# Kernel optimization log

Measured on AMD Instinct MI355X. Metric: run time of the kernel, lower is better.

The kernel has to match this reference:

```python
import jax, jax.numpy as jnp
import numpy as np

EPS = 1e-5

def _layer_norm(x, w, b):
    mu = jnp.mean(x, axis=-1, keepdims=True)
    var = jnp.mean((x - mu) ** 2, axis=-1, keepdims=True)
    return (x - mu) * jax.lax.rsqrt(var + EPS) * w + b

def setup_inputs() -> dict:
    H = 2048
    B, T = 4, 2048
    key = jax.random.key(0)
    ks = jax.random.split(key, 12)
    s = 0.02
    return {
        "hidden_state": jax.random.normal(ks[0], (B, T, H), dtype=jnp.float32),
        "ln_w": jnp.ones((H,), jnp.float32),
        "ln_b": jnp.zeros((H,), jnp.float32),
        "Wk": jax.random.normal(ks[1], (H, H), jnp.float32) * s,
        "Wv": jax.random.normal(ks[2], (H, H), jnp.float32) * s,
        "Wr": jax.random.normal(ks[3], (H, H), jnp.float32) * s,
        "Wo": jax.random.normal(ks[4], (H, H), jnp.float32) * s,
        "mix_k": jax.random.uniform(ks[5], (H,), jnp.float32),
        "mix_v": jax.random.uniform(ks[6], (H,), jnp.float32),
        "mix_r": jax.random.uniform(ks[7], (H,), jnp.float32),
        "time_decay": jax.random.normal(ks[8], (H,), jnp.float32) * 0.5,
        "current_token_weight": jax.random.normal(ks[9], (H,), jnp.float32) * 0.5,
    }

def _wkv(k, v, time_decay, curr_w):
    # k, v: [B, T, H]; max-stabilized RWKV recurrence, scanned over time.
    B, T, H = k.shape
    decay = -jnp.exp(time_decay)  # [H]
    num0 = jnp.zeros((B, H), k.dtype)
    den0 = jnp.zeros((B, H), k.dtype)
    norm0 = jnp.full((B, H), -jnp.inf, k.dtype)

    def step(carry, kv):
        num, den, norm = carry
        kt, vt = kv  # [B, H]
        ct = curr_w + kt
        cn = jnp.maximum(ct, norm)
        e_prev = jnp.exp(norm - cn)
        e_cur = jnp.exp(ct - cn)
        out = (e_prev * num + e_cur * vt) / (e_prev * den + e_cur)
        dpn = decay + norm
        new_norm = jnp.maximum(dpn, kt)
        e_d = jnp.exp(dpn - new_norm)
        e_k = jnp.exp(kt - new_norm)
        return (e_d * num + e_k * vt, e_d * den + e_k, new_norm), out

    kT = jnp.swapaxes(k, 0, 1)  # [T, B, H]
    vT = jnp.swapaxes(v, 0, 1)
    (num, den, norm), outs = jax.lax.scan(step, (num0, den0, norm0), (kT, vT))
    return jnp.swapaxes(outs, 0, 1), num, den, norm

def reference(hidden_state, ln_w, ln_b, Wk, Wv, Wr, Wo, mix_k, mix_v, mix_r,
              time_decay, current_token_weight):
    residual = hidden_state
    x = _layer_norm(hidden_state, ln_w, ln_b)  # [B, T, H]
    B, T, H = x.shape
    # shifted input: previous token (zeros for t=0 since previous_state is None)
    sx = jnp.concatenate([jnp.zeros((B, 1, H), x.dtype), x[:, :-1, :]], axis=1)
    xk = sx + mix_k * (x - sx)
    xv = sx + mix_v * (x - sx)
    xr = sx + mix_r * (x - sx)
    r = jax.nn.sigmoid(jnp.einsum('bth,oh->bto', xr, Wr))
    k = jnp.einsum('bth,oh->bto', xk, Wk)
    v = jnp.einsum('bth,oh->bto', xv, Wv)
    wkv, num, den, norm = _wkv(k, v, time_decay, current_token_weight)
    rwkv = jnp.einsum('bth,oh->bto', r * wkv, Wo)
    out = residual + rwkv
    return (out, (x[:, -1, :], num, den, norm))
```

## Files before the change

kernel.cpp:

```cpp
#include <hip/hip_runtime.h>
#include <hip/hip_bf16.h>
#include <stdint.h>

#define B_ 4
#define T_ 2048
#define H_ 2048
#define BT_ (B_ * T_)
#define BH_ (B_ * H_)
#define CH_ 32
#define CL_ (T_ / CH_)
#define NKT_ (H_ / 64)

typedef __bf16 bf16x8 __attribute__((ext_vector_type(8)));
typedef float f32x4 __attribute__((ext_vector_type(4)));

__device__ inline void async16(const void* g, void* l) {
  __builtin_amdgcn_global_load_lds(
      (__attribute__((address_space(1))) uint32_t*)(void*)(uintptr_t)g,
      (__attribute__((address_space(3))) uint32_t*)l,
      16, 0, 0);
}

__global__ __launch_bounds__(256) void cvt_bf16_kernel(
    const float* __restrict__ src, __bf16* __restrict__ dst) {
  int i = (blockIdx.x * 256 + threadIdx.x) * 8;
  const float4* s4 = (const float4*)(src + i);
  float4 a = s4[0], b = s4[1];
  bf16x8 o;
  o[0] = (__bf16)a.x; o[1] = (__bf16)a.y; o[2] = (__bf16)a.z; o[3] = (__bf16)a.w;
  o[4] = (__bf16)b.x; o[5] = (__bf16)b.y; o[6] = (__bf16)b.z; o[7] = (__bf16)b.w;
  *(bf16x8*)(dst + i) = o;
}

__global__ __launch_bounds__(256) void ln_mix_kernel(
    const float* __restrict__ h, const float* __restrict__ lnw,
    const float* __restrict__ lnb, const float* __restrict__ mk,
    const float* __restrict__ mv, const float* __restrict__ mr,
    __bf16* __restrict__ xk, __bf16* __restrict__ xv, __bf16* __restrict__ xr,
    float* __restrict__ xlast) {
  const int row = blockIdx.x;
  const int t = row & (T_ - 1);
  const int tid = threadIdx.x;
  const bool hasprev = (t != 0);

  const float4* cr = (const float4*)(h + (size_t)row * H_);
  float4 c0 = cr[tid * 2 + 0], c1 = cr[tid * 2 + 1];
  float4 p0 = {0.f, 0.f, 0.f, 0.f}, p1 = {0.f, 0.f, 0.f, 0.f};
  if (hasprev) {
    const float4* pr = (const float4*)(h + (size_t)(row - 1) * H_);
    p0 = pr[tid * 2 + 0]; p1 = pr[tid * 2 + 1];
  }
  float4 red;
  red.x = c0.x + c0.y + c0.z + c0.w + c1.x + c1.y + c1.z + c1.w;
  red.y = c0.x * c0.x + c0.y * c0.y + c0.z * c0.z + c0.w * c0.w +
          c1.x * c1.x + c1.y * c1.y + c1.z * c1.z + c1.w * c1.w;
  red.z = p0.x + p0.y + p0.z + p0.w + p1.x + p1.y + p1.z + p1.w;
  red.w = p0.x * p0.x + p0.y * p0.y + p0.z * p0.z + p0.w * p0.w +
          p1.x * p1.x + p1.y * p1.y + p1.z * p1.z + p1.w * p1.w;
  #pragma unroll
  for (int off = 32; off; off >>= 1) {
    red.x += __shfl_down(red.x, off);
    red.y += __shfl_down(red.y, off);
    red.z += __shfl_down(red.z, off);
    red.w += __shfl_down(red.w, off);
  }
  __shared__ float4 rbuf[4];
  const int lane = tid & 63, wid = tid >> 6;
  if (lane == 0) rbuf[wid] = red;
  __syncthreads();
  float4 tot;
  tot.x = rbuf[0].x + rbuf[1].x + rbuf[2].x + rbuf[3].x;
  tot.y = rbuf[0].y + rbuf[1].y + rbuf[2].y + rbuf[3].y;
  tot.z = rbuf[0].z + rbuf[1].z + rbuf[2].z + rbuf[3].z;
  tot.w = rbuf[0].w + rbuf[1].w + rbuf[2].w + rbuf[3].w;

  const float inv = 1.0f / (float)H_;
  float mu = tot.x * inv;
  float rstd = rsqrtf(fmaxf(tot.y * inv - mu * mu, 0.f) + 1e-5f);
  float mup = tot.z * inv;
  float rstdp = rsqrtf(fmaxf(tot.w * inv - mup * mup, 0.f) + 1e-5f);

  float xc[8] = {c0.x, c0.y, c0.z, c0.w, c1.x, c1.y, c1.z, c1.w};
  float xp[8] = {p0.x, p0.y, p0.z, p0.w, p1.x, p1.y, p1.z, p1.w};
  const float4* W4 = (const float4*)lnw;
  const float4* Bv4 = (const float4*)lnb;
  const float4* MK4 = (const float4*)mk;
  const float4* MV4 = (const float4*)mv;
  const float4* MR4 = (const float4*)mr;
  float4 w0 = W4[tid * 2], w1 = W4[tid * 2 + 1];
  float4 b0 = Bv4[tid * 2], b1 = Bv4[tid * 2 + 1];
  float4 k0 = MK4[tid * 2], k1 = MK4[tid * 2 + 1];
  float4 v0 = MV4[tid * 2], v1 = MV4[tid * 2 + 1];
  float4 r0 = MR4[tid * 2], r1 = MR4[tid * 2 + 1];
  float wa[8] = {w0.x, w0.y, w0.z, w0.w, w1.x, w1.y, w1.z, w1.w};
  float ba[8] = {b0.x, b0.y, b0.z, b0.w, b1.x, b1.y, b1.z, b1.w};
  float ka[8] = {k0.x, k0.y, k0.z, k0.w, k1.x, k1.y, k1.z, k1.w};
  float va[8] = {v0.x, v0.y, v0.z, v0.w, v1.x, v1.y, v1.z, v1.w};
  float ra[8] = {r0.x, r0.y, r0.z, r0.w, r1.x, r1.y, r1.z, r1.w};

  bf16x8 ok_, ov_, or_;
  float xls[8];
  #pragma unroll
  for (int e = 0; e < 8; e++) {
    float x = (xc[e] - mu) * rstd * wa[e] + ba[e];
    float sx = hasprev ? (xp[e] - mup) * rstdp * wa[e] + ba[e] : 0.f;
    ok_[e] = (__bf16)(sx + ka[e] * (x - sx));
    ov_[e] = (__bf16)(sx + va[e] * (x - sx));
    or_[e] = (__bf16)(sx + ra[e] * (x - sx));
    xls[e] = x;
  }
  size_t obase = (size_t)row * H_ + tid * 8;
  *(bf16x8*)(xk + obase) = ok_;
  *(bf16x8*)(xv + obase) = ov_;
  *(bf16x8*)(xr + obase) = or_;
  if (t == T_ - 1) {
    float* dst = xlast + (size_t)(row >> 11) * H_ + tid * 8;
    #pragma unroll
    for (int e = 0; e < 8; e++) dst[e] = xls[e];
  }
}

template <int MODE>
__global__ __launch_bounds__(512, 1) void gemm_nt4(
    const __bf16* __restrict__ A, const __bf16* __restrict__ Bw,
    float* __restrict__ outf, __bf16* __restrict__ outb,
    const float* __restrict__ resid) {
  __shared__ __align__(16) char ring[2][65536];

  const int wgid = blockIdx.x;
  const int lin = (wgid & 7) * 32 + (wgid >> 3);
  const int bm = lin >> 3;
  const int bn = lin & 7;

  const int tid = threadIdx.x;
  const int lane = tid & 63, wv = tid >> 6;
  const int wm = wv >> 2;
  const int wn = wv & 3;
  const int rr = lane & 15, q = lane >> 4;

  f32x4 acc[8][4];
  #pragma unroll
  for (int m = 0; m < 8; m++)
    #pragma unroll
    for (int n = 0; n < 4; n++) acc[m][n] = (f32x4){0.f, 0.f, 0.f, 0.f};

  const char* Ag = (const char*)A + (size_t)(bm * 256) * (H_ * 2);
  const char* Bg = (const char*)Bw + (size_t)(bn * 256) * (H_ * 2);

  const int srow = wv * 8 + (lane >> 3);
  const int scol = ((lane & 7) ^ (lane >> 3)) << 4;

  const int rsw = rr & 7;

#define STAGE_TILE(kt_, buf_)                                                   \
  {                                                                             \
    char* base_ = ring[buf_];                                                   \
    _Pragma("unroll")                                                           \
    for (int mh_ = 0; mh_ < 2; mh_++) {                                         \
      const char* Mg_ = mh_ ? Bg : Ag;                                          \
      _Pragma("unroll")                                                         \
      for (int hh_ = 0; hh_ < 2; hh_++) {                                       \
        _Pragma("unroll")                                                       \
        for (int rd_ = 0; rd_ < 2; rd_++) {                                     \
          char* dst_ = base_ + mh_ * 32768 + hh_ * 16384 + rd_ * 8192 + wv * 1024; \
          const char* src_ = Mg_ + (size_t)(hh_ * 128 + rd_ * 64 + srow) * (H_ * 2) \
                             + (kt_) * 128 + scol;                              \
          async16(src_, dst_);                                                  \
        }                                                                       \
      }                                                                         \
    }                                                                           \
  }

  STAGE_TILE(0, 0);
  asm volatile("s_waitcnt vmcnt(0)" ::: "memory");
  __builtin_amdgcn_s_barrier();

  for (int kt = 0; kt < NKT_; kt++) {
    const int cur = kt & 1, nxt = cur ^ 1;
    const char* Alds = ring[cur];
    const char* Blds = ring[cur] + 32768;

    if (kt + 1 < NKT_) STAGE_TILE(kt + 1, nxt);

    bf16x8 bfr[4][2];
    #pragma unroll
    for (int ni = 0; ni < 4; ni++)
      #pragma unroll
      for (int ks = 0; ks < 2; ks++) {
        int row_t = wn * 64 + ni * 16 + rr;
        bfr[ni][ks] = *(const bf16x8*)(Blds + row_t * 128 +
                                       (((ks * 4 + q) ^ rsw) << 4));
      }

    #pragma unroll
    for (int p = 0; p < 4; p++) {
      bf16x8 af[2][2];
      #pragma unroll
      for (int mi = 0; mi < 2; mi++)
        #pragma unroll
        for (int ks = 0; ks < 2; ks++) {
          int row_t = wm * 128 + p * 32 + mi * 16 + rr;
          af[mi][ks] = *(const bf16x8*)(Alds + row_t * 128 +
                                        (((ks * 4 + q) ^ rsw) << 4));
        }
      #pragma unroll
      for (int ks = 0; ks < 2; ks++)
        #pragma unroll
        for (int mi = 0; mi < 2; mi++)
          #pragma unroll
          for (int ni = 0; ni < 4; ni++)
            acc[p * 2 + mi][ni] = __builtin_amdgcn_mfma_f32_16x16x32_bf16(
                af[mi][ks], bfr[ni][ks], acc[p * 2 + mi][ni], 0, 0, 0);
    }

    if (kt + 1 < NKT_) {
      asm volatile("s_waitcnt vmcnt(0)" ::: "memory");
      __builtin_amdgcn_s_barrier();
    }
  }
#undef STAGE_TILE

  const int r0 = bm * 256 + wm * 128 + q * 4;
  const int c0 = bn * 256 + wn * 64 + rr;
  #pragma unroll
  for (int m = 0; m < 8; m++) {
    #pragma unroll
    for (int n = 0; n < 4; n++) {
      int col = c0 + n * 16;
      #pragma unroll
      for (int rg = 0; rg < 4; rg++) {
        int rowg = r0 + m * 16 + rg;
        size_t idx = (size_t)rowg * H_ + col;
        float vv = acc[m][n][rg];
        if (MODE == 0) {
          outf[idx] = vv;
        } else if (MODE == 1) {
          outb[idx] = (__bf16)(1.f / (1.f + __expf(-vv)));
        } else {
          outf[idx] = resid[idx] + vv;
        }
      }
    }
  }
}

__global__ __launch_bounds__(256) void wkv_pass1(
    const float* __restrict__ k, const float* __restrict__ v,
    const float* __restrict__ td,
    float* __restrict__ cs_num, float* __restrict__ cs_den,
    float* __restrict__ cs_norm) {
  const int id = blockIdx.x * 256 + threadIdx.x;
  const int c = blockIdx.y;
  const int b = id >> 11;
  const int hh = id & (H_ - 1);
  const float decay = -__expf(td[hh]);
  float num = 0.f, den = 0.f, norm = -INFINITY;

  const int UN = 16;
  for (int t0 = c * CL_; t0 < (c + 1) * CL_; t0 += UN) {
    float kk[UN], vv[UN];
    size_t base = ((size_t)b * T_ + t0) * H_ + hh;
    #pragma unroll
    for (int i = 0; i < UN; i++) {
      kk[i] = k[base + (size_t)i * H_];
      vv[i] = v[base + (size_t)i * H_];
    }
    #pragma unroll
    for (int i = 0; i < UN; i++) {
      float dpn = decay + norm;
      float nn = fmaxf(dpn, kk[i]);
      float ed = __expf(dpn - nn), ek = __expf(kk[i] - nn);
      num = ed * num + ek * vv[i];
      den = ed * den + ek;
      norm = nn;
    }
  }
  cs_num[c * BH_ + id] = num;
  cs_den[c * BH_ + id] = den;
  cs_norm[c * BH_ + id] = norm;
}

__global__ __launch_bounds__(256) void wkv_scan(
    const float* __restrict__ cs_num, const float* __restrict__ cs_den,
    const float* __restrict__ cs_norm, const float* __restrict__ td,
    float* __restrict__ px_num, float* __restrict__ px_den,
    float* __restrict__ px_norm) {
  const int id = blockIdx.x * 256 + threadIdx.x;
  const int hh = id & (H_ - 1);
  const float Lw = -__expf(td[hh]) * (float)CL_;
  float num = 0.f, den = 0.f, norm = -INFINITY;
  for (int c = 0; c < CH_; c++) {
    px_num[c * BH_ + id] = num;
    px_den[c * BH_ + id] = den;
    px_norm[c * BH_ + id] = norm;
    float n_c = cs_num[c * BH_ + id];
    float d_c = cs_den[c * BH_ + id];
    float m_c = cs_norm[c * BH_ + id];
    float sn = norm + Lw;
    float on = fmaxf(sn, m_c);
    float ea = __expf(sn - on), eb = __expf(m_c - on);
    num = ea * num + eb * n_c;
    den = ea * den + eb * d_c;
    norm = on;
  }
}

__global__ __launch_bounds__(256) void wkv_pass2(
    const float* __restrict__ k, const float* __restrict__ v,
    const __bf16* __restrict__ r, const float* __restrict__ td,
    const float* __restrict__ cw,
    const float* __restrict__ px_num, const float* __restrict__ px_den,
    const float* __restrict__ px_norm,
    __bf16* __restrict__ a, float* __restrict__ ndn) {
  const int id = blockIdx.x * 256 + threadIdx.x;
  const int c = blockIdx.y;
  const int b = id >> 11;
  const int hh = id & (H_ - 1);
  const float decay = -__expf(td[hh]);
  const float cwv = cw[hh];
  float num = px_num[c * BH_ + id];
  float den = px_den[c * BH_ + id];
  float norm = px_norm[c * BH_ + id];

  const int UN = 16;
  for (int t0 = c * CL_; t0 < (c + 1) * CL_; t0 += UN) {
    float kk[UN], vv[UN], rrv[UN];
    size_t base = ((size_t)b * T_ + t0) * H_ + hh;
    #pragma unroll
    for (int i = 0; i < UN; i++) {
      kk[i] = k[base + (size_t)i * H_];
      vv[i] = v[base + (size_t)i * H_];
      rrv[i] = (float)r[base + (size_t)i * H_];
    }
    #pragma unroll
    for (int i = 0; i < UN; i++) {
      float kt = kk[i], vt = vv[i];
      float ct = cwv + kt;
      float cn = fmaxf(ct, norm);
      float ep = __expf(norm - cn), ec = __expf(ct - cn);
      float o = (ep * num + ec * vt) / (ep * den + ec);
      a[base + (size_t)i * H_] = (__bf16)(rrv[i] * o);
      float dpn = decay + norm;
      float nn = fmaxf(dpn, kt);
      float ed = __expf(dpn - nn), ek = __expf(kt - nn);
      num = ed * num + ek * vt;
      den = ed * den + ek;
      norm = nn;
    }
  }
  if (c == CH_ - 1) {
    ndn[id] = num;
    ndn[BH_ + id] = den;
    ndn[2 * BH_ + id] = norm;
  }
}

extern "C" void kernel_launch(void* const* d_in, const int* in_sizes, int n_in,
                              void* d_out, int out_size, void* d_ws, size_t ws_size,
                              hipStream_t stream) {
  const float* h   = (const float*)d_in[0];
  const float* lnw = (const float*)d_in[1];
  const float* lnb = (const float*)d_in[2];
  const float* Wk  = (const float*)d_in[3];
  const float* Wv  = (const float*)d_in[4];
  const float* Wr  = (const float*)d_in[5];
  const float* Wo  = (const float*)d_in[6];
  const float* mk  = (const float*)d_in[7];
  const float* mv  = (const float*)d_in[8];
  const float* mr  = (const float*)d_in[9];
  const float* td  = (const float*)d_in[10];
  const float* cw  = (const float*)d_in[11];

  char* ws = (char*)d_ws;
  const size_t MB = 1048576;
  __bf16* xk   = (__bf16*)(ws);
  __bf16* xv   = (__bf16*)(ws + 32 * MB);
  __bf16* xr   = (__bf16*)(ws + 64 * MB);
  float*  kbuf = (float*)(ws + 96 * MB);
  float*  vbuf = (float*)(ws + 160 * MB);
  __bf16* Wk16 = (__bf16*)(ws + 224 * MB);
  __bf16* Wv16 = Wk16 + (size_t)H_ * H_;
  __bf16* Wr16 = Wv16 + (size_t)H_ * H_;
  __bf16* Wo16 = Wr16 + (size_t)H_ * H_;
  float* cs_num  = (float*)(ws + 64 * MB);
  float* cs_den  = cs_num + (size_t)CH_ * BH_;
  float* cs_norm = cs_den + (size_t)CH_ * BH_;
  float* px_num  = cs_norm + (size_t)CH_ * BH_;
  float* px_den  = px_num + (size_t)CH_ * BH_;
  float* px_norm = px_den + (size_t)CH_ * BH_;

  float* out  = (float*)d_out;
  float* xlast = out + (size_t)BT_ * H_;
  float* ndn   = xlast + (size_t)B_ * H_;

  const int cvt_blocks = (H_ * H_) / (256 * 8);
  cvt_bf16_kernel<<<cvt_blocks, 256, 0, stream>>>(Wk, Wk16);
  cvt_bf16_kernel<<<cvt_blocks, 256, 0, stream>>>(Wv, Wv16);
  cvt_bf16_kernel<<<cvt_blocks, 256, 0, stream>>>(Wr, Wr16);
  cvt_bf16_kernel<<<cvt_blocks, 256, 0, stream>>>(Wo, Wo16);

  ln_mix_kernel<<<BT_, 256, 0, stream>>>(h, lnw, lnb, mk, mv, mr, xk, xv, xr, xlast);

  const int gemm_blocks = (BT_ / 256) * (H_ / 256);
  gemm_nt4<0><<<gemm_blocks, 512, 0, stream>>>(xk, Wk16, kbuf, nullptr, nullptr);
  gemm_nt4<0><<<gemm_blocks, 512, 0, stream>>>(xv, Wv16, vbuf, nullptr, nullptr);
  gemm_nt4<1><<<gemm_blocks, 512, 0, stream>>>(xr, Wr16, nullptr, xv , nullptr);

  dim3 wg(BH_ / 256, CH_);
  wkv_pass1<<<wg, 256, 0, stream>>>(kbuf, vbuf, td, cs_num, cs_den, cs_norm);
  wkv_scan<<<BH_ / 256, 256, 0, stream>>>(cs_num, cs_den, cs_norm, td,
                                          px_num, px_den, px_norm);
  wkv_pass2<<<wg, 256, 0, stream>>>(kbuf, vbuf, xv, td, cw,
                                    px_num, px_den, px_norm,
                                    xk , ndn);

  gemm_nt4<2><<<gemm_blocks, 512, 0, stream>>>(xk, Wo16, out, nullptr, h);
}
```

Measured before the change: 398.8 us.

## Prefetch B tiles two stages ahead with partial vmcnt waits and MFMA priority

The GEMM now keeps a double buffer for A and a triple buffer for B. B tiles are staged two k-steps ahead and A tiles one step ahead, and the barrier waits with vmcnt(4) instead of draining every outstanding load. s_setprio is raised around the MFMA block. The goal is to hide more global-load latency behind the matrix cores, at the cost of 160KB of LDS per block instead of 128KB, with a subtle ordering dependence on outstanding loads.

```diff
diff --git a/kernel.cpp b/kernel.cpp
--- a/kernel.cpp
+++ b/kernel.cpp
@@ -121,11 +121,12 @@
 }
 
 template <int MODE>
-__global__ __launch_bounds__(512, 1) void gemm_nt4(
+__global__ __launch_bounds__(512, 1) void gemm_nt5(
     const __bf16* __restrict__ A, const __bf16* __restrict__ Bw,
     float* __restrict__ outf, __bf16* __restrict__ outb,
     const float* __restrict__ resid) {
-  __shared__ __align__(16) char ring[2][65536];
+  __shared__ __align__(16) char ldsA[2][32768];
+  __shared__ __align__(16) char ldsB[3][32768];
 
   const int wgid = blockIdx.x;
   const int lin = (wgid & 7) * 32 + (wgid >> 3);
@@ -152,35 +153,32 @@
 
   const int rsw = rr & 7;
 
-#define STAGE_TILE(kt_, buf_)                                                   \
+#define STAGE_M(Mg_, dstb_, kt_)                                                \
   {                                                                             \
-    char* base_ = ring[buf_];                                                   \
     _Pragma("unroll")                                                           \
-    for (int mh_ = 0; mh_ < 2; mh_++) {                                         \
-      const char* Mg_ = mh_ ? Bg : Ag;                                          \
+    for (int hh_ = 0; hh_ < 2; hh_++) {                                         \
       _Pragma("unroll")                                                         \
-      for (int hh_ = 0; hh_ < 2; hh_++) {                                       \
-        _Pragma("unroll")                                                       \
-        for (int rd_ = 0; rd_ < 2; rd_++) {                                     \
-          char* dst_ = base_ + mh_ * 32768 + hh_ * 16384 + rd_ * 8192 + wv * 1024; \
-          const char* src_ = Mg_ + (size_t)(hh_ * 128 + rd_ * 64 + srow) * (H_ * 2) \
-                             + (kt_) * 128 + scol;                              \
-          async16(src_, dst_);                                                  \
-        }                                                                       \
+      for (int rd_ = 0; rd_ < 2; rd_++) {                                       \
+        char* dst_ = (dstb_) + hh_ * 16384 + rd_ * 8192 + wv * 1024;            \
+        const char* src_ = (Mg_) + (size_t)(hh_ * 128 + rd_ * 64 + srow) * (H_ * 2) \
+                           + (kt_) * 128 + scol;                                \
+        async16(src_, dst_);                                                    \
       }                                                                         \
     }                                                                           \
   }
 
-  STAGE_TILE(0, 0);
-  asm volatile("s_waitcnt vmcnt(0)" ::: "memory");
+  STAGE_M(Ag, ldsA[0], 0);
+  STAGE_M(Bg, ldsB[0], 0);
+  STAGE_M(Bg, ldsB[1], 1);
+  asm volatile("s_waitcnt vmcnt(4)" ::: "memory");
   __builtin_amdgcn_s_barrier();
 
   for (int kt = 0; kt < NKT_; kt++) {
-    const int cur = kt & 1, nxt = cur ^ 1;
-    const char* Alds = ring[cur];
-    const char* Blds = ring[cur] + 32768;
-
-    if (kt + 1 < NKT_) STAGE_TILE(kt + 1, nxt);
+    const char* Alds = ldsA[kt & 1];
+    const char* Blds = ldsB[kt % 3];
+
+    if (kt + 1 < NKT_) STAGE_M(Ag, ldsA[(kt + 1) & 1], kt + 1);
+    if (kt + 2 < NKT_) STAGE_M(Bg, ldsB[(kt + 2) % 3], kt + 2);
 
     bf16x8 bfr[4][2];
     #pragma unroll
@@ -192,6 +190,7 @@
                                        (((ks * 4 + q) ^ rsw) << 4));
       }
 
+    __builtin_amdgcn_s_setprio(1);
     #pragma unroll
     for (int p = 0; p < 4; p++) {
       bf16x8 af[2][2];
@@ -212,13 +211,18 @@
             acc[p * 2 + mi][ni] = __builtin_amdgcn_mfma_f32_16x16x32_bf16(
                 af[mi][ks], bfr[ni][ks], acc[p * 2 + mi][ni], 0, 0, 0);
     }
+    __builtin_amdgcn_s_setprio(0);
 
     if (kt + 1 < NKT_) {
-      asm volatile("s_waitcnt vmcnt(0)" ::: "memory");
+      if (kt + 2 < NKT_) {
+        asm volatile("s_waitcnt vmcnt(4)" ::: "memory");
+      } else {
+        asm volatile("s_waitcnt vmcnt(0)" ::: "memory");
+      }
       __builtin_amdgcn_s_barrier();
     }
   }
-#undef STAGE_TILE
+#undef STAGE_M
 
   const int r0 = bm * 256 + wm * 128 + q * 4;
   const int c0 = bn * 256 + wn * 64 + rr;
@@ -402,9 +406,9 @@
   ln_mix_kernel<<<BT_, 256, 0, stream>>>(h, lnw, lnb, mk, mv, mr, xk, xv, xr, xlast);
 
   const int gemm_blocks = (BT_ / 256) * (H_ / 256);
-  gemm_nt4<0><<<gemm_blocks, 512, 0, stream>>>(xk, Wk16, kbuf, nullptr, nullptr);
-  gemm_nt4<0><<<gemm_blocks, 512, 0, stream>>>(xv, Wv16, vbuf, nullptr, nullptr);
-  gemm_nt4<1><<<gemm_blocks, 512, 0, stream>>>(xr, Wr16, nullptr, xv , nullptr);
+  gemm_nt5<0><<<gemm_blocks, 512, 0, stream>>>(xk, Wk16, kbuf, nullptr, nullptr);
+  gemm_nt5<0><<<gemm_blocks, 512, 0, stream>>>(xv, Wv16, vbuf, nullptr, nullptr);
+  gemm_nt5<1><<<gemm_blocks, 512, 0, stream>>>(xr, Wr16, nullptr, xv , nullptr);
 
   dim3 wg(BH_ / 256, CH_);
   wkv_pass1<<<wg, 256, 0, stream>>>(kbuf, vbuf, td, cs_num, cs_den, cs_norm);
@@ -414,5 +418,5 @@
                                     px_num, px_den, px_norm,
                                     xk , ndn);
 
-  gemm_nt4<2><<<gemm_blocks, 512, 0, stream>>>(xk, Wo16, out, nullptr, h);
-}
+  gemm_nt5<2><<<gemm_blocks, 512, 0, stream>>>(xk, Wo16, out, nullptr, h);
+}
```

Measured after the change: 467.1 us. 17.1% more time.
